# Kernel tuning notes

Hardware: AMD Instinct MI355X
Metric: run time of the kernel (lower is better)

## Reference

```python
import jax, jax.numpy as jnp
import numpy as np

E = 2048  # embed_size
H = 3     # heads (each full-width)


def setup_inputs() -> dict:
    key = jax.random.key(0)
    ks = jax.random.split(key, 6)
    B, N = 4, 2048
    x = jax.random.normal(ks[0], (B, N, E), dtype=jnp.float32)
    # torch Linear weights are [out, in]; y = x @ W.T. Stack the 3 heads.
    Wq = jax.random.normal(ks[1], (H, E, E), dtype=jnp.float32) * 0.02
    Wk = jax.random.normal(ks[2], (H, E, E), dtype=jnp.float32) * 0.02
    Wv = jax.random.normal(ks[3], (H, E, E), dtype=jnp.float32) * 0.02
    fc_w = jax.random.normal(ks[4], (E, E), dtype=jnp.float32) * 0.02
    fc_b = jax.random.normal(ks[5], (E,), dtype=jnp.float32) * 0.02
    return {"x": x, "Wq": Wq, "Wk": Wk, "Wv": Wv, "fc_w": fc_w, "fc_b": fc_b}


def reference(x, Wq, Wk, Wv, fc_w, fc_b):
    # Per-head full-width projections: [H, B, N, E]
    Q = jnp.einsum('bne,hde->hbnd', x, Wq)
    K = jnp.einsum('bne,hde->hbnd', x, Wk)
    V = jnp.einsum('bne,hde->hbnd', x, Wv)
    scale = 1.0 / jnp.sqrt(jnp.float32(E))
    # scores: [H, B, Nq, Nk]
    scores = jnp.einsum('hbnd,hbmd->hbnm', Q, K) * scale
    # Original uses torch.softmax(..., dim=1) on [B, Nq, Nk] -> query axis.
    # With leading head axis that is axis=2 here. Faithful reproduction.
    w = jax.nn.softmax(scores, axis=2)
    attn = jnp.einsum('hbnm,hbmd->hbnd', w, V)  # [H, B, N, E]
    mean = jnp.mean(attn, axis=0)               # [B, N, E]
    return mean @ fc_w.T + fc_b
```

## Files before the change

### kernel.cpp

```cpp
#include <hip/hip_runtime.h>
#include <stdint.h>

typedef __attribute__((ext_vector_type(4))) float floatx4;
typedef __bf16 bf16x8 __attribute__((ext_vector_type(8)));
typedef unsigned short ushort_t;

__device__ __forceinline__ ushort_t f2bf(float f) {
  unsigned u = __float_as_uint(f);
  u += 0x7FFFu + ((u >> 16) & 1u);
  return (ushort_t)(u >> 16);
}

__device__ __forceinline__ void gl_lds16(const void* g, void* l) {
  __builtin_amdgcn_global_load_lds(
      (__attribute__((address_space(1))) void*)g,
      (__attribute__((address_space(3))) void*)l, 16, 0, 0);
}

#define BAR() asm volatile("s_barrier" ::: "memory")
#define VM0() asm volatile("s_waitcnt vmcnt(0)" ::: "memory")

__global__ void cvt_f32_bf16(const float* __restrict__ src,
                             ushort_t* __restrict__ dst, long n) {
  long i = ((long)blockIdx.x * 256 + threadIdx.x) * 4;
  if (i >= n) return;
  float4 v = *(const float4*)(src + i);
  ushort4 o;
  o.x = f2bf(v.x); o.y = f2bf(v.y); o.z = f2bf(v.z); o.w = f2bf(v.w);
  *(ushort4*)(dst + i) = o;
}

template <int MODE>
__global__ __launch_bounds__(512, 2) void gemm256(
    const ushort_t* __restrict__ Abase, const ushort_t* __restrict__ Bbase,
    void* __restrict__ Cbase, const float* __restrict__ bias,
    int K, int lda, int ldb, int ldc,
    long strideA, long strideB, long strideC, float alpha) {
  __shared__ alignas(16) ushort_t sAB[2][2][256 * 64];

  const int z = blockIdx.z;
  const ushort_t* A = Abase + (long)z * strideA;
  const ushort_t* B = Bbase + (long)z * strideB;

  int bx, by;
  {
    const int gx = gridDim.x;
    const int nwg = gx * gridDim.y;
    const int f = blockIdx.x + gx * blockIdx.y;
    const int q = nwg >> 3, r = nwg & 7;
    const int xcd = f & 7, idx = f >> 3;
    const int fs = (xcd < r ? xcd * (q + 1) : r * (q + 1) + (xcd - r) * q) + idx;
    bx = fs % gx;
    by = fs / gx;
  }
  const int row0 = by * 256;
  const int col0 = bx * 256;

  const int tid  = threadIdx.x;
  const int lane = tid & 63;
  const int wave = tid >> 6;
  const int wm   = wave >> 2;
  const int wn   = wave & 3;

  const int fr = lane & 15;
  const int kq = lane >> 4;

  const int srow = lane >> 3;
  const int scol = ((lane & 7) ^ srow) * 8;

  const int kx0 = ((kq << 3)) ^ ((fr & 7) << 3);
  const int kx1 = ((1 << 5) | (kq << 3)) ^ ((fr & 7) << 3);

  const ushort_t* Ag = A + (long)(row0 + wave * 8 + srow) * lda + scol;
  const ushort_t* Bg = B + (long)(col0 + wave * 8 + srow) * ldb + scol;

  const floatx4 zero4 = {0.f, 0.f, 0.f, 0.f};
  floatx4 acc[8][4];
#pragma unroll
  for (int a = 0; a < 8; ++a)
#pragma unroll
    for (int b = 0; b < 4; ++b) acc[a][b] = zero4;

  const int nt = K >> 6;

  auto stageA = [&](long kk, int buf) {
#pragma unroll
    for (int i = 0; i < 4; ++i)
      gl_lds16(Ag + (long)i * 64 * lda + kk,
               &sAB[buf][0][(i * 64 + wave * 8) * 64]);
  };
  auto stageB = [&](long kk, int buf) {
#pragma unroll
    for (int i = 0; i < 4; ++i)
      gl_lds16(Bg + (long)i * 64 * ldb + kk,
               &sAB[buf][1][(i * 64 + wave * 8) * 64]);
  };

  stageA(0, 0);
  stageB(0, 0);
  VM0();
  BAR();

#define MFMA_Q(QM, QN)                                                       \
  _Pragma("unroll") for (int mi = 0; mi < 4; ++mi)                           \
  _Pragma("unroll") for (int nj = 0; nj < 2; ++nj)                           \
  _Pragma("unroll") for (int ks = 0; ks < 2; ++ks)                           \
      acc[(QM)*4 + mi][(QN)*2 + nj] = __builtin_amdgcn_mfma_f32_16x16x32_bf16( \
          af[mi][ks], bq[nj][ks], acc[(QM)*4 + mi][(QN)*2 + nj], 0, 0, 0);

  int cur = 0;
  for (int t = 0; t < nt; ++t) {
    const int nxt = cur ^ 1;
    const bool pf = (t + 1 < nt);
    const long kk = (long)(t + 1) << 6;
    const ushort_t* sA = sAB[cur][0];
    const ushort_t* sB = sAB[cur][1];
    bf16x8 af[4][2], bq[2][2];

#pragma unroll
    for (int mi = 0; mi < 4; ++mi) {
      const int rowb = (wm * 128 + mi * 16 + fr) * 64;
      af[mi][0] = *(const bf16x8*)&sA[rowb + kx0];
      af[mi][1] = *(const bf16x8*)&sA[rowb + kx1];
    }
#pragma unroll
    for (int nj = 0; nj < 2; ++nj) {
      const int rowb = (wn * 64 + nj * 16 + fr) * 64;
      bq[nj][0] = *(const bf16x8*)&sB[rowb + kx0];
      bq[nj][1] = *(const bf16x8*)&sB[rowb + kx1];
    }
    if (pf) stageA(kk, nxt);
    BAR();
    __builtin_amdgcn_s_setprio(1);
    MFMA_Q(0, 0);
    __builtin_amdgcn_s_setprio(0);
    BAR();

#pragma unroll
    for (int nj = 0; nj < 2; ++nj) {
      const int rowb = (wn * 64 + 32 + nj * 16 + fr) * 64;
      bq[nj][0] = *(const bf16x8*)&sB[rowb + kx0];
      bq[nj][1] = *(const bf16x8*)&sB[rowb + kx1];
    }
    if (pf) stageB(kk, nxt);
    BAR();
    __builtin_amdgcn_s_setprio(1);
    MFMA_Q(0, 1);
    __builtin_amdgcn_s_setprio(0);
    BAR();

#pragma unroll
    for (int mi = 0; mi < 4; ++mi) {
      const int rowb = (wm * 128 + 64 + mi * 16 + fr) * 64;
      af[mi][0] = *(const bf16x8*)&sA[rowb + kx0];
      af[mi][1] = *(const bf16x8*)&sA[rowb + kx1];
    }
    BAR();
    __builtin_amdgcn_s_setprio(1);
    MFMA_Q(1, 1);
    __builtin_amdgcn_s_setprio(0);
    BAR();

#pragma unroll
    for (int nj = 0; nj < 2; ++nj) {
      const int rowb = (wn * 64 + nj * 16 + fr) * 64;
      bq[nj][0] = *(const bf16x8*)&sB[rowb + kx0];
      bq[nj][1] = *(const bf16x8*)&sB[rowb + kx1];
    }
    BAR();
    __builtin_amdgcn_s_setprio(1);
    MFMA_Q(1, 0);
    __builtin_amdgcn_s_setprio(0);
    VM0();
    BAR();

    cur = nxt;
  }
#undef MFMA_Q

  const int ccol  = lane & 15;
  const int crow4 = (lane >> 4) * 4;

  if (MODE == 0 || MODE == 3 || MODE == 4) {
    float* C = (float*)Cbase + (long)z * strideC;
#pragma unroll
    for (int a = 0; a < 8; ++a) {
      const int rbase = row0 + wm * 128 + (a >> 2) * 64 + (a & 3) * 16 + crow4;
#pragma unroll
      for (int b = 0; b < 4; ++b) {
        const int c = col0 + wn * 64 + (b >> 1) * 32 + (b & 1) * 16 + ccol;
        const float bb = (MODE == 3) ? bias[c] : 0.f;
#pragma unroll
        for (int r = 0; r < 4; ++r) {
          const long idx = (long)(rbase + r) * ldc + c;
          float v;
          if (MODE == 3)      v = acc[a][b][r] + bb;
          else if (MODE == 4) v = C[idx] + alpha * acc[a][b][r];
          else                v = alpha * acc[a][b][r];
          C[idx] = v;
        }
      }
    }
  } else {
    ushort_t* C = (ushort_t*)Cbase;
    const long QS = strideC;
#pragma unroll
    for (int a = 0; a < 8; ++a) {
      const int rbase = row0 + wm * 128 + (a >> 2) * 64 + (a & 3) * 16 + crow4;
#pragma unroll
      for (int b = 0; b < 4; ++b) {
        const int c = col0 + wn * 64 + (b >> 1) * 32 + (b & 1) * 16 + ccol;
#pragma unroll
        for (int r = 0; r < 4; ++r) {
          const int rr = rbase + r;
          const ushort_t v = f2bf(acc[a][b][r]);
          if (c < 2048)
            C[(long)rr * 2048 + c] = v;
          else if (c < 4096)
            C[QS + (long)rr * 2048 + (c - 2048)] = v;
          else
            C[2 * QS + (long)(rr >> 11) * 4194304 + (long)(c - 4096) * 2048 +
              (rr & 2047)] = v;
        }
      }
    }
  }
}

__global__ void softmax_cols(const float* __restrict__ Sbase,
                             ushort_t* __restrict__ wbase) {
  __shared__ float rmx[8][32], rsum[8][32];
  const long zoff = (long)blockIdx.y * 4194304;
  const int tx = threadIdx.x & 31;
  const int ty = threadIdx.x >> 5;
  const int m = blockIdx.x * 32 + tx;
  const float* Sm = Sbase + zoff + m;
  const int n0 = ty * 256;

  float mx = -3.0e38f, sum = 0.f;
#pragma unroll 4
  for (int n = n0; n < n0 + 256; ++n) {
    const float v = Sm[(long)n * 2048];
    if (v > mx) {
      sum = sum * __expf(mx - v) + 1.f;
      mx = v;
    } else {
      sum += __expf(v - mx);
    }
  }
  rmx[ty][tx] = mx;
  rsum[ty][tx] = sum;
  __syncthreads();
  float gm = rmx[0][tx];
#pragma unroll
  for (int s = 1; s < 8; ++s) gm = fmaxf(gm, rmx[s][tx]);
  float gs = 0.f;
#pragma unroll
  for (int s = 0; s < 8; ++s) gs += rsum[s][tx] * __expf(rmx[s][tx] - gm);
  const float inv = 1.f / gs;

  ushort_t* wm_ = wbase + zoff + m;
#pragma unroll 4
  for (int n = n0; n < n0 + 256; ++n)
    wm_[(long)n * 2048] = f2bf(__expf(Sm[(long)n * 2048] - gm) * inv);
}

extern "C" void kernel_launch(void* const* d_in, const int* in_sizes, int n_in,
                              void* d_out, int out_size, void* d_ws,
                              size_t ws_size, hipStream_t stream) {
  const float* x   = (const float*)d_in[0];
  const float* Wq  = (const float*)d_in[1];
  const float* Wk  = (const float*)d_in[2];
  const float* Wv  = (const float*)d_in[3];
  const float* fcw = (const float*)d_in[4];
  const float* fcb = (const float*)d_in[5];
  float* out = (float*)d_out;

  char* ws = (char*)d_ws;
  size_t off = 0;
  auto alloc = [&](size_t bytes) {
    char* p = ws + off;
    off += (bytes + 255) & ~(size_t)255;
    return p;
  };
  const long SL = 4194304L;
  const dim3 blk(256);
  const dim3 blk512(512);
  const float scale = 0.022097086912079608f;

  ushort_t* xb   = (ushort_t*)alloc(33554432);
  ushort_t* fcwb = (ushort_t*)alloc(8388608);
  float* mean32 = out;
  char* loop0 = ws + off;

  cvt_f32_bf16<<<16384, blk, 0, stream>>>(x, xb, 16777216L);
  cvt_f32_bf16<<<4096, blk, 0, stream>>>(fcw, fcwb, 4194304L);

  const bool big = ws_size >= 234881024ULL;

  if (big) {
    ushort_t* Wcat = (ushort_t*)alloc(25165824);
    ushort_t* Qh   = (ushort_t*)alloc(33554432);
    ushort_t* Kh   = (ushort_t*)alloc(33554432);
    ushort_t* Vth  = (ushort_t*)alloc(33554432);
    float*    S    = (float*)alloc(67108864);
    ushort_t* wc   = Qh;
    (void)Kh; (void)Vth;

    for (int h = 0; h < 3; ++h) {
      cvt_f32_bf16<<<4096, blk, 0, stream>>>(Wq + h * SL, Wcat, SL);
      cvt_f32_bf16<<<4096, blk, 0, stream>>>(Wk + h * SL, Wcat + SL, SL);
      cvt_f32_bf16<<<4096, blk, 0, stream>>>(Wv + h * SL, Wcat + 2 * SL, SL);

      gemm256<5><<<dim3(24, 32), blk512, 0, stream>>>(
          xb, Wcat, Qh, nullptr, 2048, 2048, 2048, 2048,
          0L, 0L, 16777216L, 1.0f);
      gemm256<0><<<dim3(8, 8, 4), blk512, 0, stream>>>(
          Qh, Qh + 16777216L, S, nullptr, 2048, 2048, 2048, 2048,
          SL, SL, SL, scale);
      softmax_cols<<<dim3(64, 4), blk, 0, stream>>>(S, wc);
      if (h == 0)
        gemm256<0><<<dim3(8, 8, 4), blk512, 0, stream>>>(
            wc, Qh + 33554432L, mean32, nullptr, 2048, 2048, 2048, 2048,
            SL, SL, SL, 1.0f / 3.0f);
      else
        gemm256<4><<<dim3(8, 8, 4), blk512, 0, stream>>>(
            wc, Qh + 33554432L, mean32, nullptr, 2048, 2048, 2048, 2048,
            SL, SL, SL, 1.0f / 3.0f);
    }
  } else {
    ushort_t* Wqh  = (ushort_t*)alloc(8388608);
    ushort_t* Wkh  = (ushort_t*)alloc(8388608);
    ushort_t* Wvh  = (ushort_t*)alloc(8388608);
    ushort_t* Qhb  = (ushort_t*)alloc(8388608);
    ushort_t* Khb  = (ushort_t*)alloc(8388608);
    ushort_t* Vthb = (ushort_t*)alloc(8388608);
    float*    S    = (float*)alloc(16777216);
    ushort_t* wchb = Qhb;
    (void)Wkh; (void)Wvh; (void)Khb; (void)Vthb;

    for (int h = 0; h < 3; ++h) {
      cvt_f32_bf16<<<4096, blk, 0, stream>>>(Wq + h * SL, Wqh, SL);
      cvt_f32_bf16<<<4096, blk, 0, stream>>>(Wk + h * SL, Wqh + SL, SL);
      cvt_f32_bf16<<<4096, blk, 0, stream>>>(Wv + h * SL, Wqh + 2 * SL, SL);

      for (int b = 0; b < 4; ++b) {
        const ushort_t* xbb = xb + b * SL;
        gemm256<5><<<dim3(24, 8), blk512, 0, stream>>>(
            xbb, Wqh, Qhb, nullptr, 2048, 2048, 2048, 2048,
            0L, 0L, 4194304L, 1.0f);
        gemm256<0><<<dim3(8, 8), blk512, 0, stream>>>(
            Qhb, Qhb + SL, S, nullptr, 2048, 2048, 2048, 2048,
            0L, 0L, 0L, scale);
        softmax_cols<<<dim3(64, 1), blk, 0, stream>>>(S, wchb);
        if (h == 0)
          gemm256<0><<<dim3(8, 8), blk512, 0, stream>>>(
              wchb, Qhb + 2 * SL, mean32 + b * SL, nullptr, 2048,
              2048, 2048, 2048, 0L, 0L, 0L, 1.0f / 3.0f);
        else
          gemm256<4><<<dim3(8, 8), blk512, 0, stream>>>(
              wchb, Qhb + 2 * SL, mean32 + b * SL, nullptr, 2048,
              2048, 2048, 2048, 0L, 0L, 0L, 1.0f / 3.0f);
      }
    }
  }

  ushort_t* meanb = (ushort_t*)loop0;
  cvt_f32_bf16<<<16384, blk, 0, stream>>>(mean32, meanb, 16777216L);
  gemm256<3><<<dim3(8, 32), blk512, 0, stream>>>(
      meanb, fcwb, out, fcb, 2048, 2048, 2048, 2048,
      0L, 0L, 0L, 1.0f);
}
```

Baseline: 1.814 ms.

## Deepen GEMM prefetch to two stages with quadrant-granular LDS staging

Splits the A/B global-to-LDS staging into half-tile pieces tied to the MFMA quadrant that last reads them, so later k-tiles can be loaded into the current buffer as soon as each quadrant is consumed. The prologue fills both buffers, and the loop issues loads up to two tiles ahead, clamping the k offset at the last tile instead of branching. The end-of-iteration full vmcnt(0) wait becomes vmcnt(6), so only the loads needed for the next tile must finish. This aims to hide more global-load latency, at the cost of extra redundant loads near the tail and tighter buffer-hazard correctness.

New measurement: 1.847 ms. Within noise of the previous version (+1.8%).

```diff
diff --git a/kernel.cpp b/kernel.cpp
--- a/kernel.cpp
+++ b/kernel.cpp
@@ -19,6 +19,7 @@
 
 #define BAR() asm volatile("s_barrier" ::: "memory")
 #define VM0() asm volatile("s_waitcnt vmcnt(0)" ::: "memory")
+#define VM6() asm volatile("s_waitcnt vmcnt(6)" ::: "memory")
 
 __global__ void cvt_f32_bf16(const float* __restrict__ src,
                              ushort_t* __restrict__ dst, long n) {
@@ -71,8 +72,8 @@
   const int kx0 = ((kq << 3)) ^ ((fr & 7) << 3);
   const int kx1 = ((1 << 5) | (kq << 3)) ^ ((fr & 7) << 3);
 
-  const ushort_t* Ag = A + (long)(row0 + wave * 8 + srow) * lda + scol;
-  const ushort_t* Bg = B + (long)(col0 + wave * 8 + srow) * ldb + scol;
+  const ushort_t* Ag = A + (long)(row0 + srow) * lda + scol;
+  const ushort_t* Bg = B + (long)(col0 + srow) * ldb + scol;
 
   const floatx4 zero4 = {0.f, 0.f, 0.f, 0.f};
   floatx4 acc[8][4];
@@ -83,21 +84,24 @@
 
   const int nt = K >> 6;
 
-  auto stageA = [&](long kk, int buf) {
-#pragma unroll
-    for (int i = 0; i < 4; ++i)
-      gl_lds16(Ag + (long)i * 64 * lda + kk,
-               &sAB[buf][0][(i * 64 + wave * 8) * 64]);
+  auto stA = [&](long kk, int buf, int qm) {
+#pragma unroll
+    for (int c = 0; c < 2; ++c) {
+      const int rb = c * 128 + qm * 64 + wave * 8;
+      gl_lds16(Ag + (long)rb * lda + kk, &sAB[buf][0][rb * 64]);
+    }
   };
-  auto stageB = [&](long kk, int buf) {
-#pragma unroll
-    for (int i = 0; i < 4; ++i)
-      gl_lds16(Bg + (long)i * 64 * ldb + kk,
-               &sAB[buf][1][(i * 64 + wave * 8) * 64]);
+  auto stB = [&](long kk, int buf, int qn) {
+#pragma unroll
+    for (int c = 0; c < 2; ++c) {
+      const int g = c * 8 + wave;
+      const int rb = (g >> 2) * 64 + qn * 32 + (g & 3) * 8;
+      gl_lds16(Bg + (long)rb * ldb + kk, &sAB[buf][1][rb * 64]);
+    }
   };
 
-  stageA(0, 0);
-  stageB(0, 0);
+  stA(0, 0, 0); stA(0, 0, 1); stB(0, 0, 0); stB(0, 0, 1);
+  stA(64, 1, 0); stA(64, 1, 1); stB(64, 1, 0); stB(64, 1, 1);
   VM0();
   BAR();
 
@@ -108,11 +112,12 @@
       acc[(QM)*4 + mi][(QN)*2 + nj] = __builtin_amdgcn_mfma_f32_16x16x32_bf16( \
           af[mi][ks], bq[nj][ks], acc[(QM)*4 + mi][(QN)*2 + nj], 0, 0, 0);
 
+  const long kl = (long)(nt - 1) << 6;
   int cur = 0;
   for (int t = 0; t < nt; ++t) {
     const int nxt = cur ^ 1;
-    const bool pf = (t + 1 < nt);
-    const long kk = (long)(t + 1) << 6;
+    long k1 = (long)(t + 1) << 6; if (k1 > kl) k1 = kl;
+    long k2 = (long)(t + 2) << 6; if (k2 > kl) k2 = kl;
     const ushort_t* sA = sAB[cur][0];
     const ushort_t* sB = sAB[cur][1];
     bf16x8 af[4][2], bq[2][2];
@@ -129,7 +134,7 @@
       bq[nj][0] = *(const bf16x8*)&sB[rowb + kx0];
       bq[nj][1] = *(const bf16x8*)&sB[rowb + kx1];
     }
-    if (pf) stageA(kk, nxt);
+    stB(k1, nxt, 0);
     BAR();
     __builtin_amdgcn_s_setprio(1);
     MFMA_Q(0, 0);
@@ -142,7 +147,7 @@
       bq[nj][0] = *(const bf16x8*)&sB[rowb + kx0];
       bq[nj][1] = *(const bf16x8*)&sB[rowb + kx1];
     }
-    if (pf) stageB(kk, nxt);
+    stA(k2, cur, 0);
     BAR();
     __builtin_amdgcn_s_setprio(1);
     MFMA_Q(0, 1);
@@ -167,11 +172,13 @@
       bq[nj][0] = *(const bf16x8*)&sB[rowb + kx0];
       bq[nj][1] = *(const bf16x8*)&sB[rowb + kx1];
     }
+    stB(k2, cur, 1);
+    stA(k2, cur, 1);
     BAR();
     __builtin_amdgcn_s_setprio(1);
     MFMA_Q(1, 0);
     __builtin_amdgcn_s_setprio(0);
-    VM0();
+    VM6();
     BAR();
 
     cur = nxt;
```
